# Kernel tuning notes

Hardware: AMD Instinct MI355X
Metric: run time of the kernel (lower is better)

## Reference

```python
import jax, jax.numpy as jnp
import numpy as np

B = 8
S = 512  # seq_len


def setup_inputs() -> dict:
    key = jax.random.key(0)
    kx, kw, kb = jax.random.split(key, 3)
    x = jax.random.normal(kx, (B, S, S), dtype=jnp.float32)
    # Padded block of per-diagonal Linear weights: W[i, k, j] is weight[k, j]
    # of nn.Linear(i+1, i+1); entries with k > i or j > i are zero.
    i_d = jnp.arange(S)[:, None, None]
    k_d = jnp.arange(S)[None, :, None]
    j_d = jnp.arange(S)[None, None, :]
    wmask = ((k_d <= i_d) & (j_d <= i_d)).astype(jnp.float32)
    W = jax.random.normal(kw, (S, S, S), dtype=jnp.float32) * 0.02 * wmask
    bmask = (jnp.arange(S)[None, :] <= jnp.arange(S)[:, None]).astype(jnp.float32)
    b = jax.random.normal(kb, (S, S), dtype=jnp.float32) * 0.02 * bmask
    return {"x": x, "W": W, "b": b}


def reference(x, W, b):
    # For each anti-diagonal i (positions (r, i-r), r=0..i, with r+c=i<S):
    #   gather d = x[:, r, i-r], apply Linear_i: out = d @ W_i^T + b_i,
    #   scatter back reversed: x[:, r, i-r] = out[i-r]  =>  x[b,r,c]=out[b,r+c,c].
    S_ = x.shape[-1]
    i_idx = jnp.arange(S_)[:, None]   # diagonal index
    r_idx = jnp.arange(S_)[None, :]   # position along diagonal
    cols = (i_idx - r_idx) % S_
    valid = (r_idx <= i_idx)[None]                       # [1,S,S]
    # D[b, i, r] = x[b, r, i-r] for r<=i else 0
    D = jnp.where(valid, x[:, r_idx, cols], 0.0)         # [B,S,S]
    # Batched per-diagonal matmul: out[b,i,k] = sum_j W[i,k,j] D[b,i,j] + b[i,k]
    out = jnp.einsum('bij,ikj->bik', D, W) + b[None]     # [B,S,S]
    # Scatter back with reversal: x[b,r,c] = out[b, r+c, c] when r+c < S
    rr = jnp.arange(S_)[:, None]
    cc = jnp.arange(S_)[None, :]
    diag = rr + cc
    ok = (diag < S_)[None]
    new_x = jnp.where(ok, out[:, jnp.minimum(diag, S_ - 1), cc], x)
    return new_x
```

## Files before the change

### kernel.cpp

```cpp
#include <hip/hip_runtime.h>

#define S 512
#define NB 8
#define KT 256
#define JT 32

__global__ __launch_bounds__(256) void tail_copy_kernel(const float* __restrict__ x,
                                                        float* __restrict__ out) {
  int idx = blockIdx.x * 256 + threadIdx.x;
  int c = idx & (S - 1);
  int r = (idx >> 9) & (S - 1);
  if (r + c >= S) out[idx] = x[idx];
}

__global__ __launch_bounds__(256, 3) void diag_linear_kernel(const float* __restrict__ x,
                                                             const float* __restrict__ W,
                                                             const float* __restrict__ bias,
                                                             float* __restrict__ out) {
  __shared__ __align__(16) float WtBuf[JT * KT];
  __shared__ __align__(16) float DlBuf[S * NB];

  const int i  = (S - 1) - (int)blockIdx.x;
  const int k0 = (int)blockIdx.y * KT;
  if (k0 > i) return;

  const int tid  = threadIdx.x;
  const int wave = tid >> 6;
  const int lane = tid & 63;

  const int jend = (i + JT) & ~(JT - 1);

  for (int idx = tid; idx < jend * NB; idx += 256) {
    const int j = idx >> 3;
    const int b = idx & 7;
    DlBuf[idx] = (j <= i) ? x[b * (S * S) + j * S + (i - j)] : 0.0f;
  }

  float acc[4][NB];
#pragma unroll
  for (int m = 0; m < 4; ++m)
#pragma unroll
    for (int b = 0; b < NB; ++b) acc[m][b] = 0.0f;

  const int  k       = k0 + tid;
  const bool krow_ok = (k <= i);
  const float* wrow  = W + ((size_t)i * S + k) * S;

  float4 v[8];
#pragma unroll
  for (int q = 0; q < 8; ++q)
    v[q] = krow_ok ? *(const float4*)(wrow + 4 * q)
                   : make_float4(0.f, 0.f, 0.f, 0.f);

  for (int j0 = 0; j0 < jend; j0 += JT) {
    __syncthreads();
#pragma unroll
    for (int q = 0; q < 8; ++q) {
      WtBuf[(4 * q + 0) * KT + tid] = v[q].x;
      WtBuf[(4 * q + 1) * KT + tid] = v[q].y;
      WtBuf[(4 * q + 2) * KT + tid] = v[q].z;
      WtBuf[(4 * q + 3) * KT + tid] = v[q].w;
    }
    const int jn = j0 + JT;
    if (jn < jend && krow_ok) {
#pragma unroll
      for (int q = 0; q < 8; ++q)
        v[q] = *(const float4*)(wrow + jn + 4 * q);
    }
    __syncthreads();

#pragma unroll
    for (int u = 0; u < 8; ++u) {
      const int jl = (wave << 3) + u;
      const float4 wv = *(const float4*)&WtBuf[jl * KT + (lane << 2)];
      const float4 dA = *(const float4*)&DlBuf[(j0 + jl) * NB];
      const float4 dB = *(const float4*)&DlBuf[(j0 + jl) * NB + 4];
      const float wm[4] = {wv.x, wv.y, wv.z, wv.w};
#pragma unroll
      for (int m = 0; m < 4; ++m) {
        acc[m][0] = fmaf(wm[m], dA.x, acc[m][0]);
        acc[m][1] = fmaf(wm[m], dA.y, acc[m][1]);
        acc[m][2] = fmaf(wm[m], dA.z, acc[m][2]);
        acc[m][3] = fmaf(wm[m], dA.w, acc[m][3]);
        acc[m][4] = fmaf(wm[m], dB.x, acc[m][4]);
        acc[m][5] = fmaf(wm[m], dB.y, acc[m][5]);
        acc[m][6] = fmaf(wm[m], dB.z, acc[m][6]);
        acc[m][7] = fmaf(wm[m], dB.w, acc[m][7]);
      }
    }
  }

  __syncthreads();
  float* Racc = WtBuf;

  for (int w = 0; w < 4; ++w) {
    if (wave == w) {
#pragma unroll
      for (int b = 0; b < NB; ++b) {
        float4* p = (float4*)&Racc[b * KT + (lane << 2)];
        float4 cur = make_float4(acc[0][b], acc[1][b], acc[2][b], acc[3][b]);
        if (w != 0) {
          float4 old = *p;
          cur.x += old.x; cur.y += old.y; cur.z += old.z; cur.w += old.w;
        }
        *p = cur;
      }
    }
    __syncthreads();
  }

  if (krow_ok) {
    const float bv = bias[i * S + k];
    const int r = i - k;
#pragma unroll
    for (int b = 0; b < NB; ++b)
      out[b * (S * S) + r * S + k] = Racc[b * KT + tid] + bv;
  }
}

extern "C" void kernel_launch(void* const* d_in, const int* in_sizes, int n_in,
                              void* d_out, int out_size, void* d_ws, size_t ws_size,
                              hipStream_t stream) {
  const float* x    = (const float*)d_in[0];
  const float* W    = (const float*)d_in[1];
  const float* bias = (const float*)d_in[2];
  float* out = (float*)d_out;

  (void)d_ws; (void)ws_size; (void)in_sizes; (void)n_in; (void)out_size;

  tail_copy_kernel<<<dim3((NB * S * S) / 256), 256, 0, stream>>>(x, out);
  diag_linear_kernel<<<dim3(S, 2), 256, 0, stream>>>(x, W, bias, out);
}
```

Baseline: 655.2 us.

## Stage diagonal gather and scatter through workspace with tiled transpose kernels

Adds a gather kernel that writes the anti-diagonals of x into a contiguous [i][j][b] workspace, and a scatter kernel that writes results back to the output through a shared-memory tile. Before, the main kernel read x and wrote out with strided, uncoalesced accesses. W tile loads are also reorganised so each row is read by 8 adjacent threads as float4s, and the shared buffer uses a padded stride of 257 to avoid bank conflicts. The cost is two extra launches and an extra round trip through workspace memory.

Measured after the change: 666.8 us. About the same (+1.8%).

```diff
diff --git a/kernel.cpp b/kernel.cpp
--- a/kernel.cpp
+++ b/kernel.cpp
@@ -4,20 +4,43 @@
 #define NB 8
 #define KT 256
 #define JT 32
-
-__global__ __launch_bounds__(256) void tail_copy_kernel(const float* __restrict__ x,
-                                                        float* __restrict__ out) {
-  int idx = blockIdx.x * 256 + threadIdx.x;
-  int c = idx & (S - 1);
-  int r = (idx >> 9) & (S - 1);
-  if (r + c >= S) out[idx] = x[idx];
-}
-
-__global__ __launch_bounds__(256, 3) void diag_linear_kernel(const float* __restrict__ x,
+#define WT_STRIDE 257
+
+
+__global__ __launch_bounds__(256) void gather_diag_kernel(const float* __restrict__ x,
+                                                          float* __restrict__ Diag) {
+  __shared__ float T[32 * 32 * NB];
+  const int i0 = blockIdx.x * 32;
+  const int j0 = blockIdx.y * 32;
+  const int t  = threadIdx.x;
+  const int jl = t >> 3;
+  const int b  = t & 7;
+  const int j  = j0 + jl;
+
+  const float* xr = x + (size_t)b * (S * S) + (size_t)j * S;
+  const int cbase = i0 - j;
+#pragma unroll
+  for (int m = 0; m < 32; ++m) {
+    const int c = cbase + m;
+    T[m * (32 * NB) + jl * NB + b] = (c >= 0) ? xr[c] : 0.0f;
+  }
+  __syncthreads();
+
+  const int row0 = t >> 6;
+  const int f4   = t & 63;
+#pragma unroll
+  for (int p = 0; p < 8; ++p) {
+    const int row = p * 4 + row0;
+    const float4 v = *(const float4*)&T[row * (32 * NB) + 4 * f4];
+    *(float4*)(Diag + (size_t)(i0 + row) * (S * NB) + j0 * NB + 4 * f4) = v;
+  }
+}
+
+__global__ __launch_bounds__(256, 3) void diag_linear_kernel(const float* __restrict__ Diag,
                                                              const float* __restrict__ W,
                                                              const float* __restrict__ bias,
-                                                             float* __restrict__ out) {
-  __shared__ __align__(16) float WtBuf[JT * KT];
+                                                             float* __restrict__ Res) {
+  __shared__ __align__(16) float WtBuf[JT * WT_STRIDE];
   __shared__ __align__(16) float DlBuf[S * NB];
 
   const int i  = (S - 1) - (int)blockIdx.x;
@@ -30,10 +53,10 @@
 
   const int jend = (i + JT) & ~(JT - 1);
 
-  for (int idx = tid; idx < jend * NB; idx += 256) {
-    const int j = idx >> 3;
-    const int b = idx & 7;
-    DlBuf[idx] = (j <= i) ? x[b * (S * S) + j * S + (i - j)] : 0.0f;
+  {
+    const float4* src = (const float4*)(Diag + (size_t)i * (S * NB));
+    float4*       dst = (float4*)DlBuf;
+    for (int idx = tid; idx < jend * 2; idx += 256) dst[idx] = src[idx];
   }
 
   float acc[4][NB];
@@ -42,37 +65,42 @@
 #pragma unroll
     for (int b = 0; b < NB; ++b) acc[m][b] = 0.0f;
 
-  const int  k       = k0 + tid;
-  const bool krow_ok = (k <= i);
-  const float* wrow  = W + ((size_t)i * S + k) * S;
+  const int rsub = tid >> 3;
+  const int jsub = 4 * (tid & 7);
+  const float* wbase = W + ((size_t)i * S + (size_t)(k0 + rsub)) * S + jsub;
+
+  bool rok[8];
+#pragma unroll
+  for (int q = 0; q < 8; ++q) rok[q] = (k0 + 32 * q + rsub) <= i;
 
   float4 v[8];
 #pragma unroll
   for (int q = 0; q < 8; ++q)
-    v[q] = krow_ok ? *(const float4*)(wrow + 4 * q)
-                   : make_float4(0.f, 0.f, 0.f, 0.f);
+    v[q] = rok[q] ? *(const float4*)(wbase + (size_t)q * (32 * S))
+                  : make_float4(0.f, 0.f, 0.f, 0.f);
 
   for (int j0 = 0; j0 < jend; j0 += JT) {
     __syncthreads();
 #pragma unroll
     for (int q = 0; q < 8; ++q) {
-      WtBuf[(4 * q + 0) * KT + tid] = v[q].x;
-      WtBuf[(4 * q + 1) * KT + tid] = v[q].y;
-      WtBuf[(4 * q + 2) * KT + tid] = v[q].z;
-      WtBuf[(4 * q + 3) * KT + tid] = v[q].w;
+      const int kl = 32 * q + rsub;
+      WtBuf[(jsub + 0) * WT_STRIDE + kl] = v[q].x;
+      WtBuf[(jsub + 1) * WT_STRIDE + kl] = v[q].y;
+      WtBuf[(jsub + 2) * WT_STRIDE + kl] = v[q].z;
+      WtBuf[(jsub + 3) * WT_STRIDE + kl] = v[q].w;
     }
     const int jn = j0 + JT;
-    if (jn < jend && krow_ok) {
+    if (jn < jend) {
 #pragma unroll
       for (int q = 0; q < 8; ++q)
-        v[q] = *(const float4*)(wrow + jn + 4 * q);
+        if (rok[q]) v[q] = *(const float4*)(wbase + (size_t)q * (32 * S) + jn);
     }
     __syncthreads();
 
 #pragma unroll
     for (int u = 0; u < 8; ++u) {
       const int jl = (wave << 3) + u;
-      const float4 wv = *(const float4*)&WtBuf[jl * KT + (lane << 2)];
+      const float4 wv = *(const float4*)&WtBuf[jl * WT_STRIDE + (lane << 2)];
       const float4 dA = *(const float4*)&DlBuf[(j0 + jl) * NB];
       const float4 dB = *(const float4*)&DlBuf[(j0 + jl) * NB + 4];
       const float wm[4] = {wv.x, wv.y, wv.z, wv.w};
@@ -109,12 +137,48 @@
     __syncthreads();
   }
 
-  if (krow_ok) {
-    const float bv = bias[i * S + k];
-    const int r = i - k;
-#pragma unroll
-    for (int b = 0; b < NB; ++b)
-      out[b * (S * S) + r * S + k] = Racc[b * KT + tid] + bv;
+  {
+    float4* dst = (float4*)(Res + ((size_t)i * S + k0) * NB);
+    for (int idx = tid; idx < 512; idx += 256) {
+      const int kl = idx >> 1;
+      const int h  = (idx & 1) * 4;
+      const float bv = bias[(size_t)i * S + k0 + kl];
+      float4 o;
+      o.x = Racc[(h + 0) * KT + kl] + bv;
+      o.y = Racc[(h + 1) * KT + kl] + bv;
+      o.z = Racc[(h + 2) * KT + kl] + bv;
+      o.w = Racc[(h + 3) * KT + kl] + bv;
+      dst[idx] = o;
+    }
+  }
+}
+
+__global__ __launch_bounds__(256) void scatter_out_kernel(const float* __restrict__ x,
+                                                          const float* __restrict__ Res,
+                                                          float* __restrict__ out) {
+  __shared__ float T[32 * 32 * NB];
+  const int r0 = blockIdx.x * 32;
+  const int c0 = blockIdx.y * 32;
+  const int t  = threadIdx.x;
+  const int cl = t >> 3;
+  const int b  = t & 7;
+
+  if (r0 + c0 < S) {
+#pragma unroll 4
+    for (int p = 0; p < 32; ++p) {
+      const int ii = r0 + p + c0 + cl;
+      if (ii < S)
+        T[p * 256 + t] = Res[((size_t)ii * S + (c0 + cl)) * NB + b];
+    }
+  }
+  __syncthreads();
+
+#pragma unroll 8
+  for (int r = 0; r < 32; ++r) {
+    const int gr = r0 + r;
+    const int gc = c0 + cl;
+    const size_t o = (size_t)b * (S * S) + (size_t)gr * S + gc;
+    out[o] = (gr + gc < S) ? T[r * 256 + t] : x[o];
   }
 }
 
@@ -126,8 +190,12 @@
   const float* bias = (const float*)d_in[2];
   float* out = (float*)d_out;
 
-  (void)d_ws; (void)ws_size; (void)in_sizes; (void)n_in; (void)out_size;
-
-  tail_copy_kernel<<<dim3((NB * S * S) / 256), 256, 0, stream>>>(x, out);
-  diag_linear_kernel<<<dim3(S, 2), 256, 0, stream>>>(x, W, bias, out);
-}
+  float* Diag = (float*)d_ws;
+  float* Res  = (float*)d_ws + (size_t)S * S * NB;
+
+  (void)ws_size; (void)in_sizes; (void)n_in; (void)out_size;
+
+  gather_diag_kernel<<<dim3(S / 32, S / 32), 256, 0, stream>>>(x, Diag);
+  diag_linear_kernel<<<dim3(S, 2), 256, 0, stream>>>(Diag, W, bias, Res);
+  scatter_out_kernel<<<dim3(S / 32, S / 32), 256, 0, stream>>>(x, Res, out);
+}
```
